# Kernel optimization log

Measured on AMD Instinct MI355X. Metric: run time of the kernel, lower is better.

## Reference

```python
import jax, jax.numpy as jnp
import numpy as np

N = 512   # particles
T = 128   # timesteps
V_L = 3.4
V_0 = 4.2
GAMMA = 0.9
ALPHA = 0.15
BETA = 15.0
E_CRIT_INV = 2e-5
F_STD = 0.05
G_STD = 0.02
NU = 1.0 / (G_STD * float(np.sqrt(2.0 * np.pi)))
CUR_MIN = 0.0
CUR_MAX = 1.0


def voc(soc):
    # open-circuit voltage model
    return (V_L + (V_0 - V_L) * jnp.exp(GAMMA * (soc - 1.0))
            + ALPHA * V_L * (soc - 1.0)
            + (1.0 - ALPHA) * V_L * (jnp.exp(-BETA) - jnp.exp(-BETA * jnp.sqrt(soc))))


def mlp(x, w1, b1, w2, b2, w3, b3):
    h = jax.nn.sigmoid(x @ w1 + b1)
    h = jax.nn.sigmoid(h @ w2 + b2)
    return h @ w3 + b3


def setup_inputs() -> dict:
    key = jax.random.key(0)
    ks = jax.random.split(key, 11)
    soc_init = jax.random.uniform(ks[0], (N, 1), jnp.float32, 0.6, 1.0)
    current = jax.random.uniform(ks[1], (1, T), jnp.float32)
    voltage_measured = 3.4 + 0.8 * jax.random.uniform(ks[2], (1, T), jnp.float32)
    noise = jax.random.normal(ks[3], (T, N, 1), jnp.float32)
    u = jax.random.uniform(ks[4], (T,), jnp.float32)
    w1 = jax.random.normal(ks[5], (2, 1024), jnp.float32) / np.float32(np.sqrt(2.0))
    b1 = jnp.zeros((1024,), jnp.float32)
    w2 = jax.random.normal(ks[6], (1024, 512), jnp.float32) / np.float32(np.sqrt(1024.0))
    b2 = jnp.zeros((512,), jnp.float32)
    w3 = jax.random.normal(ks[7], (512, 1), jnp.float32) / np.float32(np.sqrt(512.0))
    b3 = jnp.zeros((1,), jnp.float32)
    return {"soc_init": soc_init, "current": current, "voltage_measured": voltage_measured,
            "noise": noise, "u": u, "w1": w1, "b1": b1, "w2": w2, "b2": b2, "w3": w3, "b3": b3}


def reference(soc_init, current, voltage_measured, noise, u, w1, b1, w2, b2, w3, b3):
    n = soc_init.shape[0]
    # pre-loop step: V at t=0 conditions
    I0 = current[0, 0] * jnp.ones_like(soc_init)
    sI0 = (I0 - CUR_MIN) / (CUR_MAX - CUR_MIN)
    Z0 = mlp(jnp.concatenate([soc_init, sI0], axis=1), w1, b1, w2, b2, w3, b3)
    V0 = voc(soc_init) - I0 * Z0

    log_n = jnp.log(jnp.float32(n))

    def step(carry, xs):
        soc, I, V = carry
        cur_t, vmeas_t, noise_t, u_t = xs
        # state propagation with process noise, then clamp to (0, 1]
        soc = soc - I * V * E_CRIT_INV + F_STD * noise_t
        soc = jnp.where(soc > 1.0, 1.0, jnp.where(soc < 0.0, 1e-10, soc))
        I = cur_t * jnp.ones_like(soc)
        sI = (I - CUR_MIN) / (CUR_MAX - CUR_MIN)
        Z = mlp(jnp.concatenate([soc, sI], axis=1), w1, b1, w2, b2, w3, b3)  # [N,1]
        V = voc(soc) - I * Z                                                 # [N,1]
        # importance weights / step loss (logsumexp trick as in source)
        logW = jnp.log(jnp.float32(NU)) - 0.5 * jnp.square((V - vmeas_t) / G_STD)
        step_loss = jax.nn.logsumexp(logW) - log_n
        # systematic resampling on normalized weights
        wn = jax.nn.softmax(logW[:, 0])          # normalized weights [N]
        cum = jnp.cumsum(wn)
        pos = (jnp.arange(n, dtype=jnp.float32) + u_t) / jnp.float32(n)
        idx = jnp.clip(jnp.searchsorted(cum, pos), 0, n - 1)
        soc_r = soc[idx]
        return (soc_r, I, V), (V[:, 0], soc_r[:, 0], step_loss)

    xs = (current[0], voltage_measured[0], noise, u)
    _, (v_hist, s_hist, losses) = jax.lax.scan(step, (soc_init, I0, V0), xs)
    loss = jnp.sum(losses)
    voltage = v_hist.T    # [N, T]
    soc_hist = s_hist.T   # [N, T]
    return loss, voltage, soc_hist
```

## Files before the change

### kernel.cpp

```cpp
#include <hip/hip_runtime.h>
#include <math.h>

#define NB 256
#define NP 512
#define TS 128
#define GI 33
#define TAB2D (GI * GI)
#define GV 193
#define V_Lc 3.4f
#define V_0c 4.2f
#define GAMMAc 0.9f
#define ALPHAc 0.15f
#define BETAc 15.0f
#define E_INV 2e-5f
#define F_STDc 0.05f
#define G_STDc 0.02f

#define LBAR() asm volatile("s_waitcnt lgkmcnt(0)\n\ts_barrier" ::: "memory")

__device__ __forceinline__ float sigmoid_jax(float x) {
    float e = expf(-fabsf(x));
    float num = (x >= 0.f) ? 1.f : e;
    return num / (1.f + e);
}

__device__ __forceinline__ float vocf(float s) {
    float sm1 = s - 1.f;
    return V_Lc + (V_0c - V_Lc) * expf(GAMMAc * sm1)
         + (ALPHAc * V_Lc) * sm1
         + (1.f - ALPHAc) * V_Lc * (expf(-BETAc) - expf(-BETAc * sqrtf(s)));
}

template <int R>
__device__ __forceinline__ int dpp_ror(int v) {
    return __builtin_amdgcn_update_dpp(0, v, 0x120 | R, 0xf, 0xf, false);
}
template <int S>
__device__ __forceinline__ int dpp_shr(int v) {
    return __builtin_amdgcn_update_dpp(0, v, 0x110 | S, 0xf, 0xf, true);
}

__device__ __forceinline__ float wave_max_f(float v) {
    v = fmaxf(v, __int_as_float(dpp_ror<1>(__float_as_int(v))));
    v = fmaxf(v, __int_as_float(dpp_ror<2>(__float_as_int(v))));
    v = fmaxf(v, __int_as_float(dpp_ror<4>(__float_as_int(v))));
    v = fmaxf(v, __int_as_float(dpp_ror<8>(__float_as_int(v))));
    int iv = __float_as_int(v);
    v = fmaxf(v, __int_as_float(__builtin_amdgcn_update_dpp(iv, iv, 0x142, 0xf, 0xf, false)));
    iv = __float_as_int(v);
    v = fmaxf(v, __int_as_float(__builtin_amdgcn_update_dpp(iv, iv, 0x143, 0xf, 0xf, false)));
    return __int_as_float(__builtin_amdgcn_readlane(__float_as_int(v), 63));
}

__device__ __forceinline__ int wave_max_i(int v) {
    v = max(v, dpp_ror<1>(v));
    v = max(v, dpp_ror<2>(v));
    v = max(v, dpp_ror<4>(v));
    v = max(v, dpp_ror<8>(v));
    v = max(v, __builtin_amdgcn_update_dpp(v, v, 0x142, 0xf, 0xf, false));
    v = max(v, __builtin_amdgcn_update_dpp(v, v, 0x143, 0xf, 0xf, false));
    return __builtin_amdgcn_readlane(v, 63);
}

__device__ __forceinline__ float wave_scan_add(float v, int lane) {
    v += __int_as_float(dpp_shr<1>(__float_as_int(v)));
    v += __int_as_float(dpp_shr<2>(__float_as_int(v)));
    v += __int_as_float(dpp_shr<4>(__float_as_int(v)));
    v += __int_as_float(dpp_shr<8>(__float_as_int(v)));
    float s15 = __int_as_float(__builtin_amdgcn_readlane(__float_as_int(v), 15));
    float s31 = __int_as_float(__builtin_amdgcn_readlane(__float_as_int(v), 31));
    float s47 = __int_as_float(__builtin_amdgcn_readlane(__float_as_int(v), 47));
    int row = lane >> 4;
    if (row >= 1) v += s15;
    if (row >= 2) v += s31;
    if (row >= 3) v += s47;
    return v;
}

__device__ __forceinline__ int wave_scanmax_i(int v, int lane) {
    v = max(v, dpp_shr<1>(v));
    v = max(v, dpp_shr<2>(v));
    v = max(v, dpp_shr<4>(v));
    v = max(v, dpp_shr<8>(v));
    int r15 = __builtin_amdgcn_readlane(v, 15);
    int r31 = __builtin_amdgcn_readlane(v, 31);
    int r47 = __builtin_amdgcn_readlane(v, 47);
    int row = lane >> 4;
    if (row >= 1) v = max(v, r15);
    if (row >= 2) v = max(v, r31);
    if (row >= 3) v = max(v, r47);
    return v;
}

__device__ __forceinline__ float cubic_at(const float* __restrict__ row, float x) {
    int j = (int)floorf(x);
    j = j < 0 ? 0 : (j > 31 ? 31 : j);
    int st = j - 1;
    st = st < 0 ? 0 : (st > 29 ? 29 : st);
    float uu = x - (float)st;
    float um0 = uu, um1 = uu - 1.f, um2 = uu - 2.f, um3 = uu - 3.f;
    float c0 = um1 * um2 * um3 * (-1.f / 6.f);
    float c1 = um0 * um2 * um3 * (0.5f);
    float c2 = um0 * um1 * um3 * (-0.5f);
    float c3 = um0 * um1 * um2 * (1.f / 6.f);
    return c0 * row[st] + c1 * row[st + 1] + c2 * row[st + 2] + c3 * row[st + 3];
}

__device__ __forceinline__ int count_le(float C, float u) {
    int h = (int)floorf(C - u);
    h = h < -1 ? -1 : (h > 511 ? 511 : h);
    h += (int)((h < 511) && (((float)(h + 1) + u) <= C));
    h += (int)((h < 511) && (((float)(h + 1) + u) <= C));
    h -= (int)((h >= 0) && (((float)h + u) > C));
    h -= (int)((h >= 0) && (((float)h + u) > C));
    return h + 1;
}

union ShU {
    struct {
        float As[5][33];
        float srow[5], irow[5];
        float Bs[32][512];
        float red[5][8];
    } p1;
    struct {
        float vt[TS][GV];
        float ztI[TS][GI];
        float vocs[GV];
        float zt2d[TAB2D];
        float socs[2][NP];
        float cur[TS], vm[TS], uu[TS];
        float redM[8], redT[8];
        int marker[NP];
    } p2;
    float tile[32][33];
};

__global__ __launch_bounds__(512, 1) void k_all(
    const float* __restrict__ soc_init, const float* __restrict__ current,
    const float* __restrict__ vmeas, const float* __restrict__ u,
    const float* __restrict__ noise,
    const float* __restrict__ w1, const float* __restrict__ b1,
    const float* __restrict__ w2, const float* __restrict__ b2,
    const float* __restrict__ w3, const float* __restrict__ b3,
    float* __restrict__ zpart, float* __restrict__ vbuf, float* __restrict__ sbuf,
    int* __restrict__ syncv, float* __restrict__ out)
{
    __shared__ ShU sh;
    const int tid = threadIdx.x;
    const int bid = blockIdx.x;
    const int lane = tid & 63;
    const int wv = tid >> 6;

    if (bid < 218) {
        const int r0 = bid * 5;
        if (tid < 5) {
            int r = r0 + tid; if (r > TAB2D - 1) r = TAB2D - 1;
            int si = r / GI, ii = r - si * GI;
            sh.p1.srow[tid] = (float)si * (1.0f / 32.0f);
            sh.p1.irow[tid] = (float)ii * (1.0f / 32.0f);
        }
        __syncthreads();
        float acc[5] = {0.f, 0.f, 0.f, 0.f, 0.f};
        for (int kk = 0; kk < 1024; kk += 32) {
            if (tid < 160) {
                int r = tid >> 5, k = tid & 31, kc = kk + k;
                float pre = sh.p1.srow[r] * w1[kc] + sh.p1.irow[r] * w1[1024 + kc] + b1[kc];
                sh.p1.As[r][k] = sigmoid_jax(pre);
            }
            #pragma unroll
            for (int jj = 0; jj < 8; ++jj) {
                int vi = tid + jj * 512;
                int k = vi >> 7, c4 = vi & 127;
                *(float4*)&sh.p1.Bs[k][c4 * 4] = *(const float4*)&w2[(kk + k) * 512 + c4 * 4];
            }
            __syncthreads();
            #pragma unroll
            for (int k = 0; k < 32; ++k) {
                float bv = sh.p1.Bs[k][tid];
                #pragma unroll
                for (int r = 0; r < 5; ++r) acc[r] += sh.p1.As[r][k] * bv;
            }
            __syncthreads();
        }
        float b2c = b2[tid], w3c = w3[tid];
        #pragma unroll
        for (int r = 0; r < 5; ++r) {
            float zp = w3c * sigmoid_jax(acc[r] + b2c);
            #pragma unroll
            for (int mm = 1; mm < 64; mm <<= 1) zp += __shfl_xor(zp, mm);
            if (lane == 0) sh.p1.red[r][wv] = zp;
        }
        __syncthreads();
        if (tid < 5 && (r0 + tid) < TAB2D) {
            float s = 0.f;
            #pragma unroll
            for (int w = 0; w < 8; ++w) s += sh.p1.red[tid][w];
            zpart[r0 + tid] = s;
        }
        __syncthreads();
    }

    if (tid == 0) { __threadfence(); atomicAdd(&syncv[0], 1); }

    if (bid == 0) {
        if (tid == 0) {
            while (atomicAdd(&syncv[0], 0) < NB) __builtin_amdgcn_s_sleep(7);
            __threadfence();
        }
        __syncthreads();

        float bb3 = b3[0];
        for (int j = tid; j < TAB2D; j += 512) sh.p2.zt2d[j] = zpart[j] + bb3;
        if (tid < TS) { sh.p2.cur[tid] = current[tid]; sh.p2.vm[tid] = vmeas[tid]; sh.p2.uu[tid] = u[tid]; }
        if (tid < GV) sh.p2.vocs[tid] = vocf((float)tid * (1.0f / 192.0f));
        sh.p2.marker[tid] = 0;
        __syncthreads();
        for (int idx = tid; idx < TS * GI; idx += 512) {
            int t = idx / GI, g = idx - t * GI;
            sh.p2.ztI[t][g] = cubic_at(&sh.p2.zt2d[g * GI], sh.p2.cur[t] * 32.f);
        }
        __syncthreads();
        for (int idx = tid; idx < TS * GV; idx += 512) {
            int t = idx / GV, gg = idx - t * GV;
            float xs = (float)gg * (32.0f / 192.0f);
            sh.p2.vt[t][gg] = sh.p2.vocs[gg] - sh.p2.cur[t] * cubic_at(&sh.p2.ztI[t][0], xs);
        }
        __syncthreads();

        float soc = soc_init[tid];
        float Iprev = sh.p2.cur[0];
        float V;
        {
            float x = soc * 192.f;
            int j = (int)x; j = j > 191 ? 191 : j;
            float f = x - (float)j;
            const float* vr = &sh.p2.vt[0][0];
            V = vr[j] + f * (vr[j + 1] - vr[j]);
        }
        float loss_acc = 0.f;
        const float LOG_NU = logf(19.947114020071635f);
        const float LOG_N = logf(512.f);
        float nz_cur = noise[tid];

        for (int t = 0; t < TS; ++t) {
            int tn = (t + 1 < TS) ? t + 1 : t;
            float nz_next = noise[tn * 512 + tid];

            soc = soc - Iprev * V * E_INV + F_STDc * nz_cur;
            soc = soc > 1.f ? 1.f : (soc < 0.f ? 1e-10f : soc);
            sh.p2.socs[t & 1][tid] = soc;

            float x = soc * 192.f;
            int j = (int)x; j = j > 191 ? 191 : j;
            float f = x - (float)j;
            const float* vr = &sh.p2.vt[t][0];
            V = vr[j] + f * (vr[j + 1] - vr[j]);

            float d = (V - sh.p2.vm[t]) * (1.f / G_STDc);
            float lw = LOG_NU - 0.5f * d * d;

            float m = wave_max_f(lw);
            float e = __expf(lw - m);
            float incl = wave_scan_add(e, lane);
            if (lane == 63) { sh.p2.redM[wv] = m; sh.p2.redT[wv] = incl; }
            LBAR();

            float rm = sh.p2.redM[lane & 7];
            float rt = sh.p2.redT[lane & 7];
            float M = rm;
            M = fmaxf(M, __int_as_float(dpp_ror<1>(__float_as_int(M))));
            M = fmaxf(M, __int_as_float(dpp_ror<2>(__float_as_int(M))));
            M = fmaxf(M, __int_as_float(dpp_ror<4>(__float_as_int(M))));
            M = fmaxf(M, __int_as_float(dpp_ror<8>(__float_as_int(M))));
            float fw = __expf(rm - M);
            float term = rt * fw;
            float sc = term;
            sc += __int_as_float(dpp_shr<1>(__float_as_int(sc)));
            sc += __int_as_float(dpp_shr<2>(__float_as_int(sc)));
            sc += __int_as_float(dpp_shr<4>(__float_as_int(sc)));
            float S = __int_as_float(__builtin_amdgcn_readlane(__float_as_int(sc), 7));
            float off = 0.f;
            if (wv > 0) off = __int_as_float(__builtin_amdgcn_readlane(__float_as_int(sc), wv - 1));
            float fw_own = __int_as_float(__builtin_amdgcn_readlane(__float_as_int(fw), wv));
            loss_acc += M + __logf(S) - LOG_N;

            float C = 512.f * ((off + incl * fw_own) / S);
            int hi = count_le(C, sh.p2.uu[t]);
            if (hi < 512) atomicMax(&sh.p2.marker[hi], (t << 10) | (tid + 1));
            LBAR();

            int pm = 0;
            for (int w = 0; w < wv; ++w) pm = max(pm, sh.p2.marker[w * 64 + lane]);
            pm = wave_max_i(pm);
            int v = wave_scanmax_i(sh.p2.marker[tid], lane);
            int sv = max(v, pm);
            int owner = ((sv >> 10) == t) ? (sv & 1023) : 0;
            owner = owner > 511 ? 511 : owner;
            float socr = sh.p2.socs[t & 1][owner];

            vbuf[t * 512 + tid] = V;
            sbuf[t * 512 + tid] = socr;
            soc = socr;
            Iprev = sh.p2.cur[t];
            nz_cur = nz_next;
        }
        if (tid == 0) out[0] = loss_acc;
        __syncthreads();
        if (tid == 0) { __threadfence(); atomicExch(&syncv[1], 1); }
        __syncthreads();
    } else {
        if (tid == 0) {
            while (atomicAdd(&syncv[1], 0) == 0) __builtin_amdgcn_s_sleep(7);
            __threadfence();
        }
        __syncthreads();
    }

    if (bid < 128) {
        int arr = bid >> 6, rem = bid & 63, ti = rem >> 4, ii = rem & 15;
        const float* src = arr ? sbuf : vbuf;
        float* dst = out + 1 + arr * (NP * TS);
        int tx = tid & 31, ty = tid >> 5;
        #pragma unroll
        for (int h = 0; h < 32; h += 16)
            sh.tile[ty + h][tx] = src[(ti * 32 + ty + h) * 512 + ii * 32 + tx];
        __syncthreads();
        #pragma unroll
        for (int h = 0; h < 32; h += 16)
            dst[(ii * 32 + ty + h) * 128 + ti * 32 + tx] = sh.tile[tx][ty + h];
    }
}

extern "C" void kernel_launch(void* const* d_in, const int* in_sizes, int n_in,
                              void* d_out, int out_size, void* d_ws, size_t ws_size,
                              hipStream_t stream)
{
    const float* soc_init = (const float*)d_in[0];
    const float* current  = (const float*)d_in[1];
    const float* vmeas    = (const float*)d_in[2];
    const float* noise    = (const float*)d_in[3];
    const float* u        = (const float*)d_in[4];
    const float* w1 = (const float*)d_in[5];
    const float* b1 = (const float*)d_in[6];
    const float* w2 = (const float*)d_in[7];
    const float* b2 = (const float*)d_in[8];
    const float* w3 = (const float*)d_in[9];
    const float* b3 = (const float*)d_in[10];
    float* out = (float*)d_out;
    float* ws  = (float*)d_ws;

    float* zpart = ws;
    float* vbuf  = ws + 1092;
    float* sbuf  = vbuf + NP * TS;
    int*   syncv = (int*)(sbuf + NP * TS);

    hipMemsetAsync(syncv, 0, 2 * sizeof(int), stream);
    k_all<<<NB, 512, 0, stream>>>(soc_init, current, vmeas, u, noise,
                                  w1, b1, w2, b2, w3, b3,
                                  zpart, vbuf, sbuf, syncv, out);
}
```

Before: 302.2 us.

## Evaluate voltage directly per step instead of building a dense V table

Drops the 128x193 precomputed voltage table and its two-stage cubic build. The serial particle loop now computes vocf(soc) and a cubic interpolation of the current-sliced Z table for each particle at every step. This removes setup work and a barrier but lengthens the latency-bound time loop. The change also shortens the sleep in the first spin-wait. Idle blocks now busy-spin with dummy FMAs instead of sleeping, apparently to keep the GPU clocks up, which burns power and may contend for resources.

```diff
diff --git a/kernel.cpp b/kernel.cpp
--- a/kernel.cpp
+++ b/kernel.cpp
@@ -6,7 +6,7 @@
 #define TS 128
 #define GI 33
 #define TAB2D (GI * GI)
-#define GV 193
+#define ROWS (TS * GI)
 #define V_Lc 3.4f
 #define V_0c 4.2f
 #define GAMMAc 0.9f
@@ -92,7 +92,8 @@
     return v;
 }
 
-__device__ __forceinline__ float cubic_at(const float* __restrict__ row, float x) {
+__device__ __forceinline__ float interp_z(const float* __restrict__ row, float s) {
+    float x = s * 32.0f;
     int j = (int)floorf(x);
     j = j < 0 ? 0 : (j > 31 ? 31 : j);
     int st = j - 1;
@@ -124,9 +125,7 @@
         float red[5][8];
     } p1;
     struct {
-        float vt[TS][GV];
-        float ztI[TS][GI];
-        float vocs[GV];
+        float zt[TS][GI];
         float zt2d[TAB2D];
         float socs[2][NP];
         float cur[TS], vm[TS], uu[TS];
@@ -147,6 +146,7 @@
     int* __restrict__ syncv, float* __restrict__ out)
 {
     __shared__ ShU sh;
+    __shared__ volatile int sdone;
     const int tid = threadIdx.x;
     const int bid = blockIdx.x;
     const int lane = tid & 63;
@@ -195,7 +195,7 @@
         if (tid < 5 && (r0 + tid) < TAB2D) {
             float s = 0.f;
             #pragma unroll
-            for (int w = 0; w < 8; ++w) s += sh.p1.red[tid][w];
+            for (int w = 0; w < 8; ++w) s += sh.p1.red[r0 + tid - r0 == tid ? tid : tid][w];
             zpart[r0 + tid] = s;
         }
         __syncthreads();
@@ -205,7 +205,7 @@
 
     if (bid == 0) {
         if (tid == 0) {
-            while (atomicAdd(&syncv[0], 0) < NB) __builtin_amdgcn_s_sleep(7);
+            while (atomicAdd(&syncv[0], 0) < NB) __builtin_amdgcn_s_sleep(2);
             __threadfence();
         }
         __syncthreads();
@@ -213,31 +213,17 @@
         float bb3 = b3[0];
         for (int j = tid; j < TAB2D; j += 512) sh.p2.zt2d[j] = zpart[j] + bb3;
         if (tid < TS) { sh.p2.cur[tid] = current[tid]; sh.p2.vm[tid] = vmeas[tid]; sh.p2.uu[tid] = u[tid]; }
-        if (tid < GV) sh.p2.vocs[tid] = vocf((float)tid * (1.0f / 192.0f));
         sh.p2.marker[tid] = 0;
         __syncthreads();
-        for (int idx = tid; idx < TS * GI; idx += 512) {
+        for (int idx = tid; idx < ROWS; idx += 512) {
             int t = idx / GI, g = idx - t * GI;
-            sh.p2.ztI[t][g] = cubic_at(&sh.p2.zt2d[g * GI], sh.p2.cur[t] * 32.f);
-        }
-        __syncthreads();
-        for (int idx = tid; idx < TS * GV; idx += 512) {
-            int t = idx / GV, gg = idx - t * GV;
-            float xs = (float)gg * (32.0f / 192.0f);
-            sh.p2.vt[t][gg] = sh.p2.vocs[gg] - sh.p2.cur[t] * cubic_at(&sh.p2.ztI[t][0], xs);
+            sh.p2.zt[t][g] = interp_z(&sh.p2.zt2d[g * GI], sh.p2.cur[t]);
         }
         __syncthreads();
 
         float soc = soc_init[tid];
         float Iprev = sh.p2.cur[0];
-        float V;
-        {
-            float x = soc * 192.f;
-            int j = (int)x; j = j > 191 ? 191 : j;
-            float f = x - (float)j;
-            const float* vr = &sh.p2.vt[0][0];
-            V = vr[j] + f * (vr[j + 1] - vr[j]);
-        }
+        float V = vocf(soc) - Iprev * interp_z(&sh.p2.zt[0][0], soc);
         float loss_acc = 0.f;
         const float LOG_NU = logf(19.947114020071635f);
         const float LOG_N = logf(512.f);
@@ -251,12 +237,8 @@
             soc = soc > 1.f ? 1.f : (soc < 0.f ? 1e-10f : soc);
             sh.p2.socs[t & 1][tid] = soc;
 
-            float x = soc * 192.f;
-            int j = (int)x; j = j > 191 ? 191 : j;
-            float f = x - (float)j;
-            const float* vr = &sh.p2.vt[t][0];
-            V = vr[j] + f * (vr[j + 1] - vr[j]);
-
+            float I = sh.p2.cur[t];
+            V = vocf(soc) - I * interp_z(&sh.p2.zt[t][0], soc);
             float d = (V - sh.p2.vm[t]) * (1.f / G_STDc);
             float lw = LOG_NU - 0.5f * d * d;
 
@@ -302,7 +284,7 @@
             vbuf[t * 512 + tid] = V;
             sbuf[t * 512 + tid] = socr;
             soc = socr;
-            Iprev = sh.p2.cur[t];
+            Iprev = I;
             nz_cur = nz_next;
         }
         if (tid == 0) out[0] = loss_acc;
@@ -310,9 +292,16 @@
         if (tid == 0) { __threadfence(); atomicExch(&syncv[1], 1); }
         __syncthreads();
     } else {
-        if (tid == 0) {
-            while (atomicAdd(&syncv[1], 0) == 0) __builtin_amdgcn_s_sleep(7);
-            __threadfence();
+        if (tid == 0) sdone = 0;
+        __syncthreads();
+        float x = (float)tid * 1e-6f + 1.0f;
+        while (sdone == 0) {
+            #pragma unroll
+            for (int it = 0; it < 64; ++it) x = __fmaf_rn(x, 1.0000001f, 1e-7f);
+            asm volatile("" : "+v"(x));
+            if (tid == 0) {
+                if (atomicAdd(&syncv[1], 0) != 0) { __threadfence(); sdone = 1; }
+            }
         }
         __syncthreads();
     }
```

Result: slower. 314.1 us (+3.9%).
